# Kernel tuning notes

Measured on AMD Instinct MI355X. Metric: run time of the kernel, lower is better.

## Reference

```python
import jax, jax.numpy as jnp
import numpy as np

NUM_HEADS_LIST = [8, 16]
HIDDEN_SIZE_LIST = [1024, 2048]
NUM_HEADS_KV = 8
MAX_HIDDEN = max(HIDDEN_SIZE_LIST)
B, T = 4, 1024
NEG = -1e9


def _rope_cos_sin(position_ids, head_dim, dtype):
    # HF-style RoPE: inv_freq over even dims, emb = cat(freqs, freqs)
    inv_freq = 1.0 / (10000.0 ** (jnp.arange(0, head_dim, 2, dtype=jnp.float32) / head_dim))
    freqs = position_ids.astype(jnp.float32)[..., None] * inv_freq  # (B,T,d/2)
    emb = jnp.concatenate([freqs, freqs], axis=-1)                  # (B,T,d)
    # unsqueeze head dim -> (B,1,T,d)
    return jnp.cos(emb).astype(dtype)[:, None], jnp.sin(emb).astype(dtype)[:, None]


def _rotate_half(x):
    d = x.shape[-1] // 2
    return jnp.concatenate([-x[..., d:], x[..., :d]], axis=-1)


def setup_inputs() -> dict:
    key = jax.random.key(0)
    k1, k2, k3, k4 = jax.random.split(key, 4)
    q_m = jax.random.normal(k1, (B, T, MAX_HIDDEN), dtype=jnp.float32)
    k_m = jax.random.normal(k2, (B, T, MAX_HIDDEN), dtype=jnp.float32)
    v_m = jax.random.normal(k3, (B, T, MAX_HIDDEN), dtype=jnp.float32)
    weights = jax.random.uniform(k4, (len(NUM_HEADS_LIST) * len(HIDDEN_SIZE_LIST),), dtype=jnp.float32)
    weights = weights / jnp.sum(weights)
    causal = jnp.tril(jnp.ones((T, T), dtype=bool))
    attention_mask = jnp.broadcast_to(
        jnp.where(causal, 0.0, NEG).astype(jnp.float32)[None, None], (B, 1, T, T)
    )
    position_ids = jnp.broadcast_to(jnp.arange(T, dtype=jnp.int64)[None], (B, T))
    return {"q_m": q_m, "k_m": k_m, "v_m": v_m, "weights": weights,
            "attention_mask": attention_mask, "position_ids": position_ids}


def reference(q_m, k_m, v_m, weights, attention_mask, position_ids):
    b, t, _ = q_m.shape
    dtype = q_m.dtype
    out = jnp.zeros((b, t, MAX_HIDDEN), dtype)
    l = 0
    for h in NUM_HEADS_LIST:
        d_max = MAX_HIDDEN // h  # padded head dim for this head-count config
        q_mix = jnp.zeros((b, h, t, d_max), dtype)
        k_mix = jnp.zeros((b, NUM_HEADS_KV, t, d_max), dtype)
        v_mix = jnp.zeros((b, NUM_HEADS_KV, t, d_max), dtype)
        for e in HIDDEN_SIZE_LIST:
            d = e // h
            q = q_m[:, :, :e].reshape(b, t, h, d).transpose(0, 2, 1, 3)                  # (b,h,t,d)
            k = k_m[:, :, :d * NUM_HEADS_KV].reshape(b, t, NUM_HEADS_KV, d).transpose(0, 2, 1, 3)
            v = v_m[:, :, :d * NUM_HEADS_KV].reshape(b, t, NUM_HEADS_KV, d).transpose(0, 2, 1, 3)
            cos, sin = _rope_cos_sin(position_ids, d, dtype)
            q = q * cos + _rotate_half(q) * sin
            k = k * cos + _rotate_half(k) * sin
            pad = ((0, 0), (0, 0), (0, 0), (0, d_max - d))
            w = weights[l]
            q_mix = q_mix + w * jnp.pad(q, pad)
            k_mix = k_mix + w * jnp.pad(k, pad)
            v_mix = v_mix + w * jnp.pad(v, pad)
            l += 1
        # GQA: repeat kv heads to match h
        n_rep = h // NUM_HEADS_KV
        kr = jnp.repeat(k_mix, n_rep, axis=1)
        vr = jnp.repeat(v_mix, n_rep, axis=1)
        scale = 1.0 / np.sqrt(d_max).astype(np.float32)
        scores = jnp.einsum('bhqd,bhkd->bhqk', q_mix, kr) * scale
        scores = scores + attention_mask[:, :, :, :t]
        att = jax.nn.softmax(scores, axis=-1)
        y = jnp.einsum('bhqk,bhkd->bhqd', att, vr)
        y = y.transpose(0, 2, 1, 3).reshape(b, t, h * d_max)  # h*d_max == MAX_HIDDEN
        out = out + y
    return out
```

## Files before the change

kernel.cpp:

```cpp
#include <hip/hip_runtime.h>
#include <math.h>

#define B_   4
#define T_   1024
#define MAXH 2048
#define NKV  8

typedef unsigned int uint;
typedef unsigned short ushort;
typedef __attribute__((ext_vector_type(8))) short bf16x8;
typedef __attribute__((ext_vector_type(4))) float f32x4;

__device__ __forceinline__ ushort f2bf(float f) {
    uint u = __float_as_uint(f);
    u += 0x7fffu + ((u >> 16) & 1u);
    return (ushort)(u >> 16);
}

__device__ __forceinline__ uint cvtpk_bf16(float lo, float hi) {
    uint r;
    asm("v_cvt_pk_bf16_f32 %0, %1, %2" : "=v"(r) : "v"(lo), "v"(hi));
    return r;
}

template<int H1>
__device__ __forceinline__ void mixqk_body(
    int bt, const float* __restrict__ src, ushort* __restrict__ dst0,
    ushort* __restrict__ dst1, const float* __restrict__ wts, float* L)
{
    const int t = bt & (T_ - 1), b = bt >> 10;
    const float* row = src + (size_t)bt * MAXH;
    const int tid = threadIdx.x;
#pragma unroll
    for (int i = 0; i < 2; i++) {
        int idx = tid + i * 256;
        *(float4*)&L[idx * 4] = *(const float4*)&row[idx * 4];
    }
    __syncthreads();
    const float w0s = wts[0], w0b = wts[1], w1s = wts[2], w1b = wts[3];
    const float tf = (float)t;
    constexpr float LG = 13.287712379549449f;

#pragma unroll
    for (int i = 0; i < 4; i++) {
        int p = tid + i * 256;
        int hh = p >> 7, jh = p & 127;
        float ab = tf * exp2f((float)jh * (-2.f * LG / 256.f));
        float sb = __sinf(ab), cb = __cosf(ab);
        float x0 = L[hh * 256 + jh], x1 = L[hh * 256 + jh + 128];
        float v0 = w0b * (x0 * cb - x1 * sb);
        float v1 = w0b * (x1 * cb + x0 * sb);
        float as = tf * exp2f((float)(jh & 63) * (-2.f * LG / 128.f));
        float ss = __sinf(as), cs = __cosf(as);
        float y  = L[hh * 128 + jh];
        float yr = (jh < 64) ? -L[hh * 128 + jh + 64] : L[hh * 128 + jh - 64];
        v0 += w0s * (y * cs + yr * ss);
        ushort* d0 = dst0 + (((size_t)b * 8 + hh) * T_ + t) * 256;
        d0[jh] = f2bf(v0); d0[jh + 128] = f2bf(v1);
    }
#pragma unroll
    for (int i = 0; i < H1 / 4; i++) {
        int p = tid + i * 256;
        int h = p >> 6, jh = p & 63;
        float ab = tf * exp2f((float)jh * (-2.f * LG / 128.f));
        float sb = __sinf(ab), cb = __cosf(ab);
        float x0 = L[h * 128 + jh], x1 = L[h * 128 + jh + 64];
        float v0 = w1b * (x0 * cb - x1 * sb);
        float v1 = w1b * (x1 * cb + x0 * sb);
        float as = tf * exp2f((float)(jh & 31) * (-2.f * LG / 64.f));
        float ss = __sinf(as), cs = __cosf(as);
        float y  = L[h * 64 + jh];
        float yr = (jh < 32) ? -L[h * 64 + jh + 32] : L[h * 64 + jh - 32];
        v0 += w1s * (y * cs + yr * ss);
        ushort* d1 = dst1 + (((size_t)b * H1 + h) * T_ + t) * 128;
        d1[jh] = f2bf(v0); d1[jh + 64] = f2bf(v1);
    }
}

template<int DMAX>
__device__ __forceinline__ void mixv_body(
    int bid, const float* __restrict__ src, ushort* __restrict__ dst,
    const float* __restrict__ wts, int wsi, int wbi, ushort* tile )
{
    constexpr int DS = DMAX / 2;
    constexpr int DDN = DMAX / 32;
    int dd = bid % DDN;  bid /= DDN;
    int tt = bid & 31;   int bk = bid >> 5;
    int b = bk >> 3, kh = bk & 7;
    int tid = threadIdx.x;
    float wb = wts[wbi], wsm = wts[wsi];

    int jloc = tid & 31;
    int j = dd * 32 + jloc;
#pragma unroll
    for (int p = 0; p < 4; p++) {
        int tl = (tid >> 5) + p * 8;
        const float* row = src + ((size_t)b * T_ + tt * 32 + tl) * MAXH;
        float v = wb * row[kh * DMAX + j];
        if (j < DS) v += wsm * row[kh * DS + j];
        tile[tl * 33 + jloc] = f2bf(v);
    }
    __syncthreads();
    int tl = tid & 31;
#pragma unroll
    for (int p = 0; p < 4; p++) {
        int jl = (tid >> 5) + p * 8;
        dst[((size_t)bk * DMAX + dd * 32 + jl) * T_ + tt * 32 + tl] = tile[tl * 33 + jl];
    }
}

__global__ __launch_bounds__(256) void mix_all(
    const float* __restrict__ q_m, const float* __restrict__ k_m, const float* __restrict__ v_m,
    const float* __restrict__ wts,
    ushort* qmix0, ushort* kmix0, ushort* vt0,
    ushort* qmix1, ushort* kmix1, ushort* vt1)
{
    __shared__ float L[2048];
    const int bid = blockIdx.x;
    if (bid < 4096) {
        mixqk_body<16>(bid, q_m, qmix0, qmix1, wts, L);
    } else if (bid < 8192) {
        mixqk_body<8>(bid - 4096, k_m, kmix0, kmix1, wts, L);
    } else if (bid < 16384) {
        mixv_body<256>(bid - 8192, v_m, vt0, wts, 0, 1, (ushort*)L);
    } else {
        mixv_body<128>(bid - 16384, v_m, vt1, wts, 2, 3, (ushort*)L);
    }
}

template<int NC, int NSUB, int RS, int NQ>
__device__ __forceinline__ void attn_inst(
    const bf16x8* qf, f32x4* acc, f32x4* accl,
    const ushort* lds, int ksbase, int vtbase,
    float scale2, int qw, int kt32, int qtr, int l16)
{
    const bool full = (kt32 + 31) <= qw;
    f32x4 s0[NQ], s1[NQ];
#pragma unroll
    for (int qi = 0; qi < NQ; qi++) { s0[qi] = (f32x4){0.f,0.f,0.f,0.f}; s1[qi] = (f32x4){0.f,0.f,0.f,0.f}; }

    __builtin_amdgcn_s_setprio(1);
#pragma unroll
    for (int c = 0; c < NC; c++) {
        int ch = ((c * 4 + qtr) ^ (l16 & 7)) * 8;
        bf16x8 k0 = *(const bf16x8*)&lds[ksbase + l16 * RS + ch];
        bf16x8 k1 = *(const bf16x8*)&lds[ksbase + (16 + l16) * RS + ch];
#pragma unroll
        for (int qi = 0; qi < NQ; qi++) {
            s0[qi] = __builtin_amdgcn_mfma_f32_16x16x32_bf16(k0, qf[qi * NC + c], s0[qi], 0, 0, 0);
            s1[qi] = __builtin_amdgcn_mfma_f32_16x16x32_bf16(k1, qf[qi * NC + c], s1[qi], 0, 0, 0);
        }
    }
    __builtin_amdgcn_s_setprio(0);

    bf16x8 pa[NQ];
    const bool lohalf = (qtr < 2);
    const bool evengrp = !(qtr & 1);
#pragma unroll
    for (int qi = 0; qi < NQ; qi++) {
        float p0[4], p1[4];
#pragma unroll
        for (int rr = 0; rr < 4; rr++) {
            p0[rr] = exp2f(s0[qi][rr] * scale2);
            p1[rr] = exp2f(s1[qi][rr] * scale2);
            if (!full) {
                int qq = qw + l16;
                if (kt32 + qtr * 4 + rr > qq)      p0[rr] = 0.f;
                if (kt32 + 16 + qtr * 4 + rr > qq) p1[rr] = 0.f;
            }
        }
        uint u0 = cvtpk_bf16(p0[0], p0[1]);
        uint u1 = cvtpk_bf16(p0[2], p0[3]);
        uint u2 = cvtpk_bf16(p1[0], p1[1]);
        uint u3 = cvtpk_bf16(p1[2], p1[3]);
        uint su0 = __shfl_xor(u0, 32), su1 = __shfl_xor(u1, 32);
        uint su2 = __shfl_xor(u2, 32), su3 = __shfl_xor(u3, 32);
        uint X1 = lohalf ? u0 : su2;
        uint Y1 = lohalf ? u1 : su3;
        uint X2 = lohalf ? su0 : u2;
        uint Y2 = lohalf ? su1 : u3;
        uint sX1 = __shfl_xor(X1, 16), sY1 = __shfl_xor(Y1, 16);
        uint sX2 = __shfl_xor(X2, 16), sY2 = __shfl_xor(Y2, 16);
        union { uint4 w; bf16x8 v; } cvt;
        cvt.w.x = evengrp ? X1  : sX2;
        cvt.w.y = evengrp ? Y1  : sY2;
        cvt.w.z = evengrp ? sX1 : X2;
        cvt.w.w = evengrp ? sY1 : Y2;
        pa[qi] = cvt.v;
    }

    bf16x8 ones;
#pragma unroll
    for (int j = 0; j < 8; j++) ones[j] = (short)0x3f80;
    __builtin_amdgcn_s_setprio(1);
#pragma unroll
    for (int s = 0; s < NSUB; s++) {
        bf16x8 vb = *(const bf16x8*)&lds[vtbase + (s * 16 + l16) * 32 + ((qtr ^ (l16 & 3)) * 8)];
#pragma unroll
        for (int qi = 0; qi < NQ; qi++)
            acc[qi * NSUB + s] = __builtin_amdgcn_mfma_f32_16x16x32_bf16(pa[qi], vb, acc[qi * NSUB + s], 0, 0, 0);
    }
#pragma unroll
    for (int qi = 0; qi < NQ; qi++)
        accl[qi] = __builtin_amdgcn_mfma_f32_16x16x32_bf16(pa[qi], ones, accl[qi], 0, 0, 0);
    __builtin_amdgcn_s_setprio(0);
}

__global__ __launch_bounds__(512, 2) void attn_fused(
    const ushort* __restrict__ qmix0, const ushort* __restrict__ kmix0, const ushort* __restrict__ vt0,
    const ushort* __restrict__ qmix1, const ushort* __restrict__ kmix1, const ushort* __restrict__ vt1,
    float* __restrict__ out)
{
    __shared__ alignas(16) ushort lds[24576];
    constexpr int KS0 = 0, KS1 = 8192, VT0 = 12288, VT1 = 20480;

    const int bid = blockIdx.x;
    const int half = bid >> 8;
    const int ipair = (bid >> 5) & 7;
    const int idx = bid & 31;
    const int b = idx >> 3, kh = idx & 7;
    const int qt = half ? ipair : 15 - ipair;

    const int tid = threadIdx.x;
    const int wid = tid >> 6, lane = tid & 63;
    const int qtr = lane >> 4, l16 = lane & 15;
    const int cfg = wid >> 2;
    const int w4 = wid & 3;

    const ushort* kg0 = kmix0 + ((size_t)b * NKV + kh) * T_ * 256;
    const ushort* vg0 = vt0   + ((size_t)b * NKV + kh) * 256 * T_;
    const ushort* kg1 = kmix1 + ((size_t)b * NKV + kh) * T_ * 128;
    const ushort* vg1 = vt1   + ((size_t)b * NKV + kh) * 128 * T_;

    const int k0r0 = tid >> 5,         k0c0 = tid & 31;
    const int k0r1 = (tid + 512) >> 5, k0c1 = (tid + 512) & 31;
    const int v0d0 = tid >> 2,         v0c0 = tid & 3;
    const int v0d1 = (tid + 512) >> 2, v0c1 = (tid + 512) & 3;
    const int k1r = tid >> 4, k1c = tid & 15;
    const int v1d = tid >> 2, v1c = tid & 3;

    const int nkt = 2 * qt + 2;
    const int qw = qt * 64 + w4 * 16;

    bf16x8 qf[8];
    if (cfg == 0) {
        const ushort* qb = qmix0 + (((size_t)b * 8 + kh) * T_ + qw + l16) * 256 + qtr * 8;
#pragma unroll
        for (int c = 0; c < 8; c++) qf[c] = *(const bf16x8*)(qb + c * 32);
    } else {
#pragma unroll
        for (int hI = 0; hI < 2; hI++) {
            const ushort* qb = qmix1 + (((size_t)b * 16 + 2 * kh + hI) * T_ + qw + l16) * 128 + qtr * 8;
#pragma unroll
            for (int c = 0; c < 4; c++) qf[hI * 4 + c] = *(const bf16x8*)(qb + c * 32);
        }
    }

    f32x4 acc[16];
    f32x4 accl[2] = {{0.f,0.f,0.f,0.f},{0.f,0.f,0.f,0.f}};
#pragma unroll
    for (int s = 0; s < 16; s++) acc[s] = (f32x4){0.f,0.f,0.f,0.f};

    const float scale2_0 = 0.0625f * 1.4426950408889634f;
    const float scale2_1 = 0.08838834764831845f * 1.4426950408889634f;

    uint4 k0a, k0b, v0a, v0b, k1a, v1a;
#define ISSUE(kt_) do {                                                              \
        k0a = *(const uint4*)(kg0 + (size_t)((kt_) * 32 + k0r0) * 256 + k0c0 * 8);   \
        k0b = *(const uint4*)(kg0 + (size_t)((kt_) * 32 + k0r1) * 256 + k0c1 * 8);   \
        v0a = *(const uint4*)(vg0 + (size_t)v0d0 * T_ + (kt_) * 32 + v0c0 * 8);      \
        v0b = *(const uint4*)(vg0 + (size_t)v0d1 * T_ + (kt_) * 32 + v0c1 * 8);      \
        k1a = *(const uint4*)(kg1 + (size_t)((kt_) * 32 + k1r) * 128 + k1c * 8);     \
        v1a = *(const uint4*)(vg1 + (size_t)v1d * T_ + (kt_) * 32 + v1c * 8);        \
    } while (0)

    ISSUE(0);
    for (int kt = 0; kt < nkt; kt++) {
        asm volatile("s_barrier" ::: "memory");
        *(uint4*)&lds[KS0 + k0r0 * 256 + ((k0c0 ^ (k0r0 & 7)) * 8)] = k0a;
        *(uint4*)&lds[KS0 + k0r1 * 256 + ((k0c1 ^ (k0r1 & 7)) * 8)] = k0b;
        *(uint4*)&lds[VT0 + v0d0 * 32 + ((v0c0 ^ (v0d0 & 3)) * 8)] = v0a;
        *(uint4*)&lds[VT0 + v0d1 * 32 + ((v0c1 ^ (v0d1 & 3)) * 8)] = v0b;
        *(uint4*)&lds[KS1 + k1r * 128 + ((k1c ^ (k1r & 7)) * 8)] = k1a;
        *(uint4*)&lds[VT1 + v1d * 32 + ((v1c ^ (v1d & 3)) * 8)] = v1a;
        if (kt + 1 < nkt) ISSUE(kt + 1);
        asm volatile("s_waitcnt lgkmcnt(0)" ::: "memory");
        asm volatile("s_barrier" ::: "memory");

        const int kt32 = kt * 32;
        if (kt32 > qw + 15) continue;

        if (cfg == 0) {
            attn_inst<8, 16, 256, 1>(qf, acc, accl, lds, KS0, VT0,
                                     scale2_0, qw, kt32, qtr, l16);
        } else {
            attn_inst<4, 8, 128, 2>(qf, acc, accl, lds, KS1, VT1,
                                    scale2_1, qw, kt32, qtr, l16);
        }
    }
#undef ISSUE

    if (cfg == 0) {
        float linv[4];
#pragma unroll
        for (int rr = 0; rr < 4; rr++) linv[rr] = 1.f / accl[0][rr];
        float* ob = out + ((size_t)b * T_ + qw) * MAXH + kh * 256;
#pragma unroll
        for (int s = 0; s < 16; s++)
#pragma unroll
            for (int rr = 0; rr < 4; rr++)
                ob[(size_t)(qtr * 4 + rr) * MAXH + s * 16 + l16] = acc[s][rr] * linv[rr];
    }
    __syncthreads();
    if (cfg == 1) {
        float linva[4], linvb[4];
#pragma unroll
        for (int rr = 0; rr < 4; rr++) { linva[rr] = 1.f / accl[0][rr]; linvb[rr] = 1.f / accl[1][rr]; }
        float* ob = out + ((size_t)b * T_ + qw) * MAXH + kh * 256;
#pragma unroll
        for (int s = 0; s < 8; s++)
#pragma unroll
            for (int rr = 0; rr < 4; rr++)
                ob[(size_t)(qtr * 4 + rr) * MAXH + s * 16 + l16] += acc[s][rr] * linva[rr];
#pragma unroll
        for (int s = 0; s < 8; s++)
#pragma unroll
            for (int rr = 0; rr < 4; rr++)
                ob[(size_t)(qtr * 4 + rr) * MAXH + 128 + s * 16 + l16] += acc[8 + s][rr] * linvb[rr];
    }
}

extern "C" void kernel_launch(void* const* d_in, const int* in_sizes, int n_in,
                              void* d_out, int out_size, void* d_ws, size_t ws_size,
                              hipStream_t stream) {
    const float* q_m = (const float*)d_in[0];
    const float* k_m = (const float*)d_in[1];
    const float* v_m = (const float*)d_in[2];
    const float* wts = (const float*)d_in[3];
    float* out = (float*)d_out;
    ushort* ws = (ushort*)d_ws;

    ushort* qmix0 = ws;
    ushort* kmix0 = ws + 8388608u;
    ushort* vt0   = ws + 16777216u;
    ushort* qmix1 = ws + 25165824u;
    ushort* kmix1 = ws + 33554432u;
    ushort* vt1   = ws + 37748736u;

    mix_all<<<dim3(20480), dim3(256), 0, stream>>>(q_m, k_m, v_m, wts,
                                                   qmix0, kmix0, vt0, qmix1, kmix1, vt1);
    attn_fused<<<dim3(512), dim3(512), 0, stream>>>(qmix0, kmix0, vt0, qmix1, kmix1, vt1, out);
}
```

Measured before the change: 134.3 us.

## Split KV tiles across two wave groups per block and merge partial accumulators via LDS

Doubles the block to 1024 threads as two 512-thread groups. Each group processes alternating KV tiles in its own LDS buffer, and the partial output and row-sum accumulators are then reduced through LDS before the final store. The goal is to shorten the serial KV loop per query tile and add more parallel work per CU. In exchange it adds a cross-group reduction and extra barriers, doubles LDS use, and drops the launch bound of 2 blocks per CU. With 1024 threads per block, register pressure may also force spills, since the accumulators are large.

New measurement: 405.9 us. +202.2%, slower.

```diff
diff --git a/kernel.cpp b/kernel.cpp
--- a/kernel.cpp
+++ b/kernel.cpp
@@ -206,12 +206,13 @@
     __builtin_amdgcn_s_setprio(0);
 }
 
-__global__ __launch_bounds__(512, 2) void attn_fused(
+__global__ __launch_bounds__(1024) void attn_fused(
     const ushort* __restrict__ qmix0, const ushort* __restrict__ kmix0, const ushort* __restrict__ vt0,
     const ushort* __restrict__ qmix1, const ushort* __restrict__ kmix1, const ushort* __restrict__ vt1,
     float* __restrict__ out)
 {
-    __shared__ alignas(16) ushort lds[24576];
+    __shared__ alignas(16) ushort lds[49152];
+    constexpr int GSZ = 24576;
     constexpr int KS0 = 0, KS1 = 8192, VT0 = 12288, VT1 = 20480;
 
     const int bid = blockIdx.x;
@@ -222,24 +223,30 @@
     const int qt = half ? ipair : 15 - ipair;
 
     const int tid = threadIdx.x;
-    const int wid = tid >> 6, lane = tid & 63;
+    const int wid = tid >> 6;
+    const int grp = wid >> 3;
+    const int wl  = wid & 7;
+    const int gtid = tid & 511;
+    const int lane = tid & 63;
     const int qtr = lane >> 4, l16 = lane & 15;
-    const int cfg = wid >> 2;
-    const int w4 = wid & 3;
+    const int cfg = wl >> 2;
+    const int w4 = wl & 3;
+    const int lbase = grp * GSZ;
 
     const ushort* kg0 = kmix0 + ((size_t)b * NKV + kh) * T_ * 256;
     const ushort* vg0 = vt0   + ((size_t)b * NKV + kh) * 256 * T_;
     const ushort* kg1 = kmix1 + ((size_t)b * NKV + kh) * T_ * 128;
     const ushort* vg1 = vt1   + ((size_t)b * NKV + kh) * 128 * T_;
 
-    const int k0r0 = tid >> 5,         k0c0 = tid & 31;
-    const int k0r1 = (tid + 512) >> 5, k0c1 = (tid + 512) & 31;
-    const int v0d0 = tid >> 2,         v0c0 = tid & 3;
-    const int v0d1 = (tid + 512) >> 2, v0c1 = (tid + 512) & 3;
-    const int k1r = tid >> 4, k1c = tid & 15;
-    const int v1d = tid >> 2, v1c = tid & 3;
+    const int k0r0 = gtid >> 5,         k0c0 = gtid & 31;
+    const int k0r1 = (gtid + 512) >> 5, k0c1 = (gtid + 512) & 31;
+    const int v0d0 = gtid >> 2,         v0c0 = gtid & 3;
+    const int v0d1 = (gtid + 512) >> 2, v0c1 = (gtid + 512) & 3;
+    const int k1r = gtid >> 4, k1c = gtid & 15;
+    const int v1d = gtid >> 2, v1c = gtid & 3;
 
     const int nkt = 2 * qt + 2;
+    const int niter = qt + 1;
     const int qw = qt * 64 + w4 * 16;
 
     bf16x8 qf[8];
@@ -274,33 +281,63 @@
         v1a = *(const uint4*)(vg1 + (size_t)v1d * T_ + (kt_) * 32 + v1c * 8);        \
     } while (0)
 
-    ISSUE(0);
-    for (int kt = 0; kt < nkt; kt++) {
+    ISSUE(grp);
+    for (int j = 0; j < niter; j++) {
+        const int kt = 2 * j + grp;
         asm volatile("s_barrier" ::: "memory");
-        *(uint4*)&lds[KS0 + k0r0 * 256 + ((k0c0 ^ (k0r0 & 7)) * 8)] = k0a;
-        *(uint4*)&lds[KS0 + k0r1 * 256 + ((k0c1 ^ (k0r1 & 7)) * 8)] = k0b;
-        *(uint4*)&lds[VT0 + v0d0 * 32 + ((v0c0 ^ (v0d0 & 3)) * 8)] = v0a;
-        *(uint4*)&lds[VT0 + v0d1 * 32 + ((v0c1 ^ (v0d1 & 3)) * 8)] = v0b;
-        *(uint4*)&lds[KS1 + k1r * 128 + ((k1c ^ (k1r & 7)) * 8)] = k1a;
-        *(uint4*)&lds[VT1 + v1d * 32 + ((v1c ^ (v1d & 3)) * 8)] = v1a;
-        if (kt + 1 < nkt) ISSUE(kt + 1);
+        *(uint4*)&lds[lbase + KS0 + k0r0 * 256 + ((k0c0 ^ (k0r0 & 7)) * 8)] = k0a;
+        *(uint4*)&lds[lbase + KS0 + k0r1 * 256 + ((k0c1 ^ (k0r1 & 7)) * 8)] = k0b;
+        *(uint4*)&lds[lbase + VT0 + v0d0 * 32 + ((v0c0 ^ (v0d0 & 3)) * 8)] = v0a;
+        *(uint4*)&lds[lbase + VT0 + v0d1 * 32 + ((v0c1 ^ (v0d1 & 3)) * 8)] = v0b;
+        *(uint4*)&lds[lbase + KS1 + k1r * 128 + ((k1c ^ (k1r & 7)) * 8)] = k1a;
+        *(uint4*)&lds[lbase + VT1 + v1d * 32 + ((v1c ^ (v1d & 3)) * 8)] = v1a;
+        if (j + 1 < niter) ISSUE(kt + 2);
         asm volatile("s_waitcnt lgkmcnt(0)" ::: "memory");
         asm volatile("s_barrier" ::: "memory");
 
         const int kt32 = kt * 32;
-        if (kt32 > qw + 15) continue;
-
-        if (cfg == 0) {
-            attn_inst<8, 16, 256, 1>(qf, acc, accl, lds, KS0, VT0,
-                                     scale2_0, qw, kt32, qtr, l16);
-        } else {
-            attn_inst<4, 8, 128, 2>(qf, acc, accl, lds, KS1, VT1,
-                                    scale2_1, qw, kt32, qtr, l16);
+        if (kt32 <= qw + 15) {
+            if (cfg == 0) {
+                attn_inst<8, 16, 256, 1>(qf, acc, accl, lds, lbase + KS0, lbase + VT0,
+                                         scale2_0, qw, kt32, qtr, l16);
+            } else {
+                attn_inst<4, 8, 128, 2>(qf, acc, accl, lds, lbase + KS1, lbase + VT1,
+                                        scale2_1, qw, kt32, qtr, l16);
+            }
         }
     }
 #undef ISSUE
 
-    if (cfg == 0) {
+    float* ldsF = (float*)lds;
+#pragma unroll
+    for (int r = 0; r < 2; r++) {
+        __syncthreads();
+        if (grp == 1 && (wl >> 2) == r) {
+            float* dst = &ldsF[(wl & 3) * 4608 + lane * 72];
+#pragma unroll
+            for (int s = 0; s < 16; s++)
+#pragma unroll
+                for (int rr = 0; rr < 4; rr++) dst[s * 4 + rr] = acc[s][rr];
+#pragma unroll
+            for (int qi = 0; qi < 2; qi++)
+#pragma unroll
+                for (int rr = 0; rr < 4; rr++) dst[64 + qi * 4 + rr] = accl[qi][rr];
+        }
+        __syncthreads();
+        if (grp == 0 && (wl >> 2) == r) {
+            const float* src = &ldsF[(wl & 3) * 4608 + lane * 72];
+#pragma unroll
+            for (int s = 0; s < 16; s++)
+#pragma unroll
+                for (int rr = 0; rr < 4; rr++) acc[s][rr] += src[s * 4 + rr];
+#pragma unroll
+            for (int qi = 0; qi < 2; qi++)
+#pragma unroll
+                for (int rr = 0; rr < 4; rr++) accl[qi][rr] += src[64 + qi * 4 + rr];
+        }
+    }
+
+    if (grp == 0 && cfg == 0) {
         float linv[4];
 #pragma unroll
         for (int rr = 0; rr < 4; rr++) linv[rr] = 1.f / accl[0][rr];
@@ -312,7 +349,7 @@
                 ob[(size_t)(qtr * 4 + rr) * MAXH + s * 16 + l16] = acc[s][rr] * linv[rr];
     }
     __syncthreads();
-    if (cfg == 1) {
+    if (grp == 0 && cfg == 1) {
         float linva[4], linvb[4];
 #pragma unroll
         for (int rr = 0; rr < 4; rr++) { linva[rr] = 1.f / accl[0][rr]; linvb[rr] = 1.f / accl[1][rr]; }
@@ -349,5 +386,5 @@
 
     mix_all<<<dim3(20480), dim3(256), 0, stream>>>(q_m, k_m, v_m, wts,
                                                    qmix0, kmix0, vt0, qmix1, kmix1, vt1);
-    attn_fused<<<dim3(512), dim3(512), 0, stream>>>(qmix0, kmix0, vt0, qmix1, kmix1, vt1, out);
-}
+    attn_fused<<<dim3(512), dim3(1024), 0, stream>>>(qmix0, kmix0, vt0, qmix1, kmix1, vt1, out);
+}
```

## Double-buffer K/V tiles in LDS to use one barrier per iteration

Applied to the files above, without the earlier changes.

Doubles the LDS allocation so the next K/V tile is written into the alternate buffer after computing on the current one. The loop drops from two barriers per iteration to one, and global loads for tile j+1 stay in flight during compute on tile j. In exchange, LDS use doubles to about 96KB and launch bounds drop to one block per CU, which halves occupancy from 16 to 8 waves per CU and may expose more latency.

New measurement: 133.4 us. About the same (-0.7%).

```diff
diff --git a/kernel.cpp b/kernel.cpp
--- a/kernel.cpp
+++ b/kernel.cpp
@@ -206,12 +206,13 @@
     __builtin_amdgcn_s_setprio(0);
 }
 
-__global__ __launch_bounds__(512, 2) void attn_fused(
+__global__ __launch_bounds__(512, 1) void attn_fused(
     const ushort* __restrict__ qmix0, const ushort* __restrict__ kmix0, const ushort* __restrict__ vt0,
     const ushort* __restrict__ qmix1, const ushort* __restrict__ kmix1, const ushort* __restrict__ vt1,
     float* __restrict__ out)
 {
-    __shared__ alignas(16) ushort lds[24576];
+    __shared__ alignas(16) ushort lds[49152];
+    constexpr int BSZ = 24576;
     constexpr int KS0 = 0, KS1 = 8192, VT0 = 12288, VT1 = 20480;
 
     const int bid = blockIdx.x;
@@ -273,32 +274,43 @@
         k1a = *(const uint4*)(kg1 + (size_t)((kt_) * 32 + k1r) * 128 + k1c * 8);     \
         v1a = *(const uint4*)(vg1 + (size_t)v1d * T_ + (kt_) * 32 + v1c * 8);        \
     } while (0)
+#define WRITE(base_) do {                                                            \
+        *(uint4*)&lds[(base_) + KS0 + k0r0 * 256 + ((k0c0 ^ (k0r0 & 7)) * 8)] = k0a; \
+        *(uint4*)&lds[(base_) + KS0 + k0r1 * 256 + ((k0c1 ^ (k0r1 & 7)) * 8)] = k0b; \
+        *(uint4*)&lds[(base_) + VT0 + v0d0 * 32 + ((v0c0 ^ (v0d0 & 3)) * 8)] = v0a;  \
+        *(uint4*)&lds[(base_) + VT0 + v0d1 * 32 + ((v0c1 ^ (v0d1 & 3)) * 8)] = v0b;  \
+        *(uint4*)&lds[(base_) + KS1 + k1r * 128 + ((k1c ^ (k1r & 7)) * 8)] = k1a;    \
+        *(uint4*)&lds[(base_) + VT1 + v1d * 32 + ((v1c ^ (v1d & 3)) * 8)] = v1a;     \
+    } while (0)
 
     ISSUE(0);
-    for (int kt = 0; kt < nkt; kt++) {
+    WRITE(0);
+    asm volatile("s_waitcnt lgkmcnt(0)" ::: "memory");
+    asm volatile("s_barrier" ::: "memory");
+
+    for (int j = 0; j < nkt; j++) {
+        const int lbase = (j & 1) * BSZ;
+        const bool more = (j + 1 < nkt);
+        if (more) ISSUE(j + 1);
+
+        const int kt32 = j * 32;
+        if (kt32 <= qw + 15) {
+            if (cfg == 0) {
+                attn_inst<8, 16, 256, 1>(qf, acc, accl, lds, lbase + KS0, lbase + VT0,
+                                         scale2_0, qw, kt32, qtr, l16);
+            } else {
+                attn_inst<4, 8, 128, 2>(qf, acc, accl, lds, lbase + KS1, lbase + VT1,
+                                        scale2_1, qw, kt32, qtr, l16);
+            }
+        }
+        if (more) {
+            WRITE((~j & 1) * BSZ);
+            asm volatile("s_waitcnt lgkmcnt(0)" ::: "memory");
+        }
         asm volatile("s_barrier" ::: "memory");
-        *(uint4*)&lds[KS0 + k0r0 * 256 + ((k0c0 ^ (k0r0 & 7)) * 8)] = k0a;
-        *(uint4*)&lds[KS0 + k0r1 * 256 + ((k0c1 ^ (k0r1 & 7)) * 8)] = k0b;
-        *(uint4*)&lds[VT0 + v0d0 * 32 + ((v0c0 ^ (v0d0 & 3)) * 8)] = v0a;
-        *(uint4*)&lds[VT0 + v0d1 * 32 + ((v0c1 ^ (v0d1 & 3)) * 8)] = v0b;
-        *(uint4*)&lds[KS1 + k1r * 128 + ((k1c ^ (k1r & 7)) * 8)] = k1a;
-        *(uint4*)&lds[VT1 + v1d * 32 + ((v1c ^ (v1d & 3)) * 8)] = v1a;
-        if (kt + 1 < nkt) ISSUE(kt + 1);
-        asm volatile("s_waitcnt lgkmcnt(0)" ::: "memory");
-        asm volatile("s_barrier" ::: "memory");
-
-        const int kt32 = kt * 32;
-        if (kt32 > qw + 15) continue;
-
-        if (cfg == 0) {
-            attn_inst<8, 16, 256, 1>(qf, acc, accl, lds, KS0, VT0,
-                                     scale2_0, qw, kt32, qtr, l16);
-        } else {
-            attn_inst<4, 8, 128, 2>(qf, acc, accl, lds, KS1, VT1,
-                                    scale2_1, qw, kt32, qtr, l16);
-        }
     }
 #undef ISSUE
+#undef WRITE
 
     if (cfg == 0) {
         float linv[4];
```

## Process 64-key tiles per iteration in fused attention instead of 32

Applied to the files above, without the earlier changes.

The attention loop now stages 64 keys of K and V^T per iteration, halving the number of barrier-separated iterations and global-load issue rounds. Each wave computes four 16-key score groups and two PV MFMA passes per tile. LDS doubles to 96 KB and launch bounds drop to one block per SIMD group, so occupancy falls. Waves whose query rows sit entirely before the tile no longer skip it; they rely on masking instead, which adds some wasted work on diagonal tiles.

Measured after the change: 181.7 us. 1.35x slower.

```diff
diff --git a/kernel.cpp b/kernel.cpp
--- a/kernel.cpp
+++ b/kernel.cpp
@@ -21,6 +21,28 @@
     uint r;
     asm("v_cvt_pk_bf16_f32 %0, %1, %2" : "=v"(r) : "v"(lo), "v"(hi));
     return r;
+}
+
+__device__ __forceinline__ bf16x8 p_exchange(const float* p0, const float* p1,
+                                             bool lohalf, bool evengrp) {
+    uint u0 = cvtpk_bf16(p0[0], p0[1]);
+    uint u1 = cvtpk_bf16(p0[2], p0[3]);
+    uint u2 = cvtpk_bf16(p1[0], p1[1]);
+    uint u3 = cvtpk_bf16(p1[2], p1[3]);
+    uint su0 = __shfl_xor(u0, 32), su1 = __shfl_xor(u1, 32);
+    uint su2 = __shfl_xor(u2, 32), su3 = __shfl_xor(u3, 32);
+    uint X1 = lohalf ? u0 : su2;
+    uint Y1 = lohalf ? u1 : su3;
+    uint X2 = lohalf ? su0 : u2;
+    uint Y2 = lohalf ? su1 : u3;
+    uint sX1 = __shfl_xor(X1, 16), sY1 = __shfl_xor(Y1, 16);
+    uint sX2 = __shfl_xor(X2, 16), sY2 = __shfl_xor(Y2, 16);
+    union { uint4 w; bf16x8 v; } cvt;
+    cvt.w.x = evengrp ? X1  : sX2;
+    cvt.w.y = evengrp ? Y1  : sY2;
+    cvt.w.z = evengrp ? sX1 : X2;
+    cvt.w.w = evengrp ? sY1 : Y2;
+    return cvt.v;
 }
 
 template<int H1>
@@ -129,15 +151,17 @@
 }
 
 template<int NC, int NSUB, int RS, int NQ>
-__device__ __forceinline__ void attn_inst(
+__device__ __forceinline__ void attn_inst64(
     const bf16x8* qf, f32x4* acc, f32x4* accl,
     const ushort* lds, int ksbase, int vtbase,
-    float scale2, int qw, int kt32, int qtr, int l16)
-{
-    const bool full = (kt32 + 31) <= qw;
-    f32x4 s0[NQ], s1[NQ];
-#pragma unroll
-    for (int qi = 0; qi < NQ; qi++) { s0[qi] = (f32x4){0.f,0.f,0.f,0.f}; s1[qi] = (f32x4){0.f,0.f,0.f,0.f}; }
+    float scale2, int qw, int kt64, int qtr, int l16)
+{
+    const bool full = (kt64 + 63) <= qw;
+    f32x4 s[4][NQ];
+#pragma unroll
+    for (int g = 0; g < 4; g++)
+#pragma unroll
+        for (int qi = 0; qi < NQ; qi++) s[g][qi] = (f32x4){0.f,0.f,0.f,0.f};
 
     __builtin_amdgcn_s_setprio(1);
 #pragma unroll
@@ -145,74 +169,86 @@
         int ch = ((c * 4 + qtr) ^ (l16 & 7)) * 8;
         bf16x8 k0 = *(const bf16x8*)&lds[ksbase + l16 * RS + ch];
         bf16x8 k1 = *(const bf16x8*)&lds[ksbase + (16 + l16) * RS + ch];
+        bf16x8 k2 = *(const bf16x8*)&lds[ksbase + (32 + l16) * RS + ch];
+        bf16x8 k3 = *(const bf16x8*)&lds[ksbase + (48 + l16) * RS + ch];
 #pragma unroll
         for (int qi = 0; qi < NQ; qi++) {
-            s0[qi] = __builtin_amdgcn_mfma_f32_16x16x32_bf16(k0, qf[qi * NC + c], s0[qi], 0, 0, 0);
-            s1[qi] = __builtin_amdgcn_mfma_f32_16x16x32_bf16(k1, qf[qi * NC + c], s1[qi], 0, 0, 0);
+            s[0][qi] = __builtin_amdgcn_mfma_f32_16x16x32_bf16(k0, qf[qi * NC + c], s[0][qi], 0, 0, 0);
+            s[1][qi] = __builtin_amdgcn_mfma_f32_16x16x32_bf16(k1, qf[qi * NC + c], s[1][qi], 0, 0, 0);
+            s[2][qi] = __builtin_amdgcn_mfma_f32_16x16x32_bf16(k2, qf[qi * NC + c], s[2][qi], 0, 0, 0);
+            s[3][qi] = __builtin_amdgcn_mfma_f32_16x16x32_bf16(k3, qf[qi * NC + c], s[3][qi], 0, 0, 0);
         }
     }
     __builtin_amdgcn_s_setprio(0);
 
-    bf16x8 pa[NQ];
+    bf16x8 pa0[NQ], pa1[NQ];
     const bool lohalf = (qtr < 2);
     const bool evengrp = !(qtr & 1);
+    const int qq = qw + l16;
 #pragma unroll
     for (int qi = 0; qi < NQ; qi++) {
-        float p0[4], p1[4];
-#pragma unroll
-        for (int rr = 0; rr < 4; rr++) {
-            p0[rr] = exp2f(s0[qi][rr] * scale2);
-            p1[rr] = exp2f(s1[qi][rr] * scale2);
-            if (!full) {
-                int qq = qw + l16;
-                if (kt32 + qtr * 4 + rr > qq)      p0[rr] = 0.f;
-                if (kt32 + 16 + qtr * 4 + rr > qq) p1[rr] = 0.f;
+        {
+            float p0[4], p1[4];
+#pragma unroll
+            for (int rr = 0; rr < 4; rr++) {
+                p0[rr] = exp2f(s[0][qi][rr] * scale2);
+                p1[rr] = exp2f(s[1][qi][rr] * scale2);
+                if (!full) {
+                    int key = kt64 + qtr * 4 + rr;
+                    if (key > qq)      p0[rr] = 0.f;
+                    if (key + 16 > qq) p1[rr] = 0.f;
+                }
             }
-        }
-        uint u0 = cvtpk_bf16(p0[0], p0[1]);
-        uint u1 = cvtpk_bf16(p0[2], p0[3]);
-        uint u2 = cvtpk_bf16(p1[0], p1[1]);
-        uint u3 = cvtpk_bf16(p1[2], p1[3]);
-        uint su0 = __shfl_xor(u0, 32), su1 = __shfl_xor(u1, 32);
-        uint su2 = __shfl_xor(u2, 32), su3 = __shfl_xor(u3, 32);
-        uint X1 = lohalf ? u0 : su2;
-        uint Y1 = lohalf ? u1 : su3;
-        uint X2 = lohalf ? su0 : u2;
-        uint Y2 = lohalf ? su1 : u3;
-        uint sX1 = __shfl_xor(X1, 16), sY1 = __shfl_xor(Y1, 16);
-        uint sX2 = __shfl_xor(X2, 16), sY2 = __shfl_xor(Y2, 16);
-        union { uint4 w; bf16x8 v; } cvt;
-        cvt.w.x = evengrp ? X1  : sX2;
-        cvt.w.y = evengrp ? Y1  : sY2;
-        cvt.w.z = evengrp ? sX1 : X2;
-        cvt.w.w = evengrp ? sY1 : Y2;
-        pa[qi] = cvt.v;
+            pa0[qi] = p_exchange(p0, p1, lohalf, evengrp);
+        }
+        {
+            float p0[4], p1[4];
+#pragma unroll
+            for (int rr = 0; rr < 4; rr++) {
+                p0[rr] = exp2f(s[2][qi][rr] * scale2);
+                p1[rr] = exp2f(s[3][qi][rr] * scale2);
+                if (!full) {
+                    int key = kt64 + 32 + qtr * 4 + rr;
+                    if (key > qq)      p0[rr] = 0.f;
+                    if (key + 16 > qq) p1[rr] = 0.f;
+                }
+            }
+            pa1[qi] = p_exchange(p0, p1, lohalf, evengrp);
+        }
     }
 
     bf16x8 ones;
 #pragma unroll
     for (int j = 0; j < 8; j++) ones[j] = (short)0x3f80;
+    const int vch0 = (qtr ^ (l16 & 7)) * 8;
+    const int vch1 = ((4 + qtr) ^ (l16 & 7)) * 8;
     __builtin_amdgcn_s_setprio(1);
 #pragma unroll
-    for (int s = 0; s < NSUB; s++) {
-        bf16x8 vb = *(const bf16x8*)&lds[vtbase + (s * 16 + l16) * 32 + ((qtr ^ (l16 & 3)) * 8)];
-#pragma unroll
-        for (int qi = 0; qi < NQ; qi++)
-            acc[qi * NSUB + s] = __builtin_amdgcn_mfma_f32_16x16x32_bf16(pa[qi], vb, acc[qi * NSUB + s], 0, 0, 0);
-    }
-#pragma unroll
-    for (int qi = 0; qi < NQ; qi++)
-        accl[qi] = __builtin_amdgcn_mfma_f32_16x16x32_bf16(pa[qi], ones, accl[qi], 0, 0, 0);
+    for (int s2 = 0; s2 < NSUB; s2++) {
+        const int d = s2 * 16 + l16;
+        bf16x8 vb0 = *(const bf16x8*)&lds[vtbase + d * 64 + vch0];
+        bf16x8 vb1 = *(const bf16x8*)&lds[vtbase + d * 64 + vch1];
+#pragma unroll
+        for (int qi = 0; qi < NQ; qi++) {
+            acc[qi * NSUB + s2] = __builtin_amdgcn_mfma_f32_16x16x32_bf16(pa0[qi], vb0, acc[qi * NSUB + s2], 0, 0, 0);
+            acc[qi * NSUB + s2] = __builtin_amdgcn_mfma_f32_16x16x32_bf16(pa1[qi], vb1, acc[qi * NSUB + s2], 0, 0, 0);
+        }
+    }
+#pragma unroll
+    for (int qi = 0; qi < NQ; qi++) {
+        accl[qi] = __builtin_amdgcn_mfma_f32_16x16x32_bf16(pa0[qi], ones, accl[qi], 0, 0, 0);
+        accl[qi] = __builtin_amdgcn_mfma_f32_16x16x32_bf16(pa1[qi], ones, accl[qi], 0, 0, 0);
+    }
     __builtin_amdgcn_s_setprio(0);
 }
 
-__global__ __launch_bounds__(512, 2) void attn_fused(
+__global__ __launch_bounds__(512, 1) void attn_fused(
     const ushort* __restrict__ qmix0, const ushort* __restrict__ kmix0, const ushort* __restrict__ vt0,
     const ushort* __restrict__ qmix1, const ushort* __restrict__ kmix1, const ushort* __restrict__ vt1,
     float* __restrict__ out)
 {
-    __shared__ alignas(16) ushort lds[24576];
-    constexpr int KS0 = 0, KS1 = 8192, VT0 = 12288, VT1 = 20480;
+    __shared__ alignas(16) ushort lds[49152];
+    constexpr int KS0 = 0, VT0 = 16384, KS1 = 32768, VT1 = 40960;
 
     const int bid = blockIdx.x;
     const int half = bid >> 8;
@@ -232,14 +268,14 @@
     const ushort* kg1 = kmix1 + ((size_t)b * NKV + kh) * T_ * 128;
     const ushort* vg1 = vt1   + ((size_t)b * NKV + kh) * 128 * T_;
 
-    const int k0r0 = tid >> 5,         k0c0 = tid & 31;
-    const int k0r1 = (tid + 512) >> 5, k0c1 = (tid + 512) & 31;
-    const int v0d0 = tid >> 2,         v0c0 = tid & 3;
-    const int v0d1 = (tid + 512) >> 2, v0c1 = (tid + 512) & 3;
-    const int k1r = tid >> 4, k1c = tid & 15;
-    const int v1d = tid >> 2, v1c = tid & 3;
-
-    const int nkt = 2 * qt + 2;
+    const int a0 = tid >> 5, c0 = tid & 31;
+    const int d0 = tid >> 3, cv0 = tid & 7;
+    const int a1 = tid >> 4, c1 = tid & 15;
+    const int sw_k0 = (c0 ^ (a0 & 7)) * 8;
+    const int sw_v0 = (cv0 ^ (d0 & 7)) * 8;
+    const int sw_k1 = (c1 ^ (a1 & 7)) * 8;
+
+    const int niter = qt + 1;
     const int qw = qt * 64 + w4 * 16;
 
     bf16x8 qf[8];
@@ -264,41 +300,49 @@
     const float scale2_0 = 0.0625f * 1.4426950408889634f;
     const float scale2_1 = 0.08838834764831845f * 1.4426950408889634f;
 
-    uint4 k0a, k0b, v0a, v0b, k1a, v1a;
-#define ISSUE(kt_) do {                                                              \
-        k0a = *(const uint4*)(kg0 + (size_t)((kt_) * 32 + k0r0) * 256 + k0c0 * 8);   \
-        k0b = *(const uint4*)(kg0 + (size_t)((kt_) * 32 + k0r1) * 256 + k0c1 * 8);   \
-        v0a = *(const uint4*)(vg0 + (size_t)v0d0 * T_ + (kt_) * 32 + v0c0 * 8);      \
-        v0b = *(const uint4*)(vg0 + (size_t)v0d1 * T_ + (kt_) * 32 + v0c1 * 8);      \
-        k1a = *(const uint4*)(kg1 + (size_t)((kt_) * 32 + k1r) * 128 + k1c * 8);     \
-        v1a = *(const uint4*)(vg1 + (size_t)v1d * T_ + (kt_) * 32 + v1c * 8);        \
-    } while (0)
+    uint4 k0g[4], v0g[4], k1g[2], v1g[2];
+#define ISSUE(kb_) do {                                                                     \
+        _Pragma("unroll")                                                                   \
+        for (int i = 0; i < 4; i++) {                                                       \
+            k0g[i] = *(const uint4*)(kg0 + (size_t)((kb_) + a0 + i * 16) * 256 + c0 * 8);   \
+            v0g[i] = *(const uint4*)(vg0 + (size_t)(d0 + i * 64) * T_ + (kb_) + cv0 * 8);   \
+        }                                                                                   \
+        _Pragma("unroll")                                                                   \
+        for (int i = 0; i < 2; i++) {                                                       \
+            k1g[i] = *(const uint4*)(kg1 + (size_t)((kb_) + a1 + i * 32) * 128 + c1 * 8);   \
+            v1g[i] = *(const uint4*)(vg1 + (size_t)(d0 + i * 64) * T_ + (kb_) + cv0 * 8);   \
+        } } while (0)
+#define WRITE() do {                                                                        \
+        _Pragma("unroll")                                                                   \
+        for (int i = 0; i < 4; i++) {                                                       \
+            *(uint4*)&lds[KS0 + (a0 + i * 16) * 256 + sw_k0] = k0g[i];                      \
+            *(uint4*)&lds[VT0 + (d0 + i * 64) * 64 + sw_v0] = v0g[i];                       \
+        }                                                                                   \
+        _Pragma("unroll")                                                                   \
+        for (int i = 0; i < 2; i++) {                                                       \
+            *(uint4*)&lds[KS1 + (a1 + i * 32) * 128 + sw_k1] = k1g[i];                      \
+            *(uint4*)&lds[VT1 + (d0 + i * 64) * 64 + sw_v0] = v1g[i];                       \
+        } } while (0)
 
     ISSUE(0);
-    for (int kt = 0; kt < nkt; kt++) {
+    for (int j = 0; j < niter; j++) {
         asm volatile("s_barrier" ::: "memory");
-        *(uint4*)&lds[KS0 + k0r0 * 256 + ((k0c0 ^ (k0r0 & 7)) * 8)] = k0a;
-        *(uint4*)&lds[KS0 + k0r1 * 256 + ((k0c1 ^ (k0r1 & 7)) * 8)] = k0b;
-        *(uint4*)&lds[VT0 + v0d0 * 32 + ((v0c0 ^ (v0d0 & 3)) * 8)] = v0a;
-        *(uint4*)&lds[VT0 + v0d1 * 32 + ((v0c1 ^ (v0d1 & 3)) * 8)] = v0b;
-        *(uint4*)&lds[KS1 + k1r * 128 + ((k1c ^ (k1r & 7)) * 8)] = k1a;
-        *(uint4*)&lds[VT1 + v1d * 32 + ((v1c ^ (v1d & 3)) * 8)] = v1a;
-        if (kt + 1 < nkt) ISSUE(kt + 1);
+        WRITE();
+        if (j + 1 < niter) ISSUE((j + 1) * 64);
         asm volatile("s_waitcnt lgkmcnt(0)" ::: "memory");
         asm volatile("s_barrier" ::: "memory");
 
-        const int kt32 = kt * 32;
-        if (kt32 > qw + 15) continue;
-
+        const int kt64 = j * 64;
         if (cfg == 0) {
-            attn_inst<8, 16, 256, 1>(qf, acc, accl, lds, KS0, VT0,
-                                     scale2_0, qw, kt32, qtr, l16);
+            attn_inst64<8, 16, 256, 1>(qf, acc, accl, lds, KS0, VT0,
+                                       scale2_0, qw, kt64, qtr, l16);
         } else {
-            attn_inst<4, 8, 128, 2>(qf, acc, accl, lds, KS1, VT1,
-                                    scale2_1, qw, kt32, qtr, l16);
+            attn_inst64<4, 8, 128, 2>(qf, acc, accl, lds, KS1, VT1,
+                                      scale2_1, qw, kt64, qtr, l16);
         }
     }
 #undef ISSUE
+#undef WRITE
 
     if (cfg == 0) {
         float linv[4];
```
